# Kernel optimization log

Measured on AMD Instinct MI355X. Metric: run time of the kernel, lower is better.

## Reference

```python
import jax, jax.numpy as jnp
import numpy as np

N_RAYS = 32768
N_SAMPLES = 1048576
HID = 64
STEP = 0.0005


def _mlp(x, W1, b1, W2, b2, W3, b3):
    h = jax.nn.relu(x @ W1 + b1)
    h = jax.nn.relu(h @ W2 + b2)
    return h @ W3 + b3


def setup_inputs() -> dict:
    key = jax.random.key(0)
    ks = jax.random.split(key, 12)
    rays_o = jax.random.normal(ks[0], (N_RAYS, 3), jnp.float32)
    rays_d = jax.random.normal(ks[1], (N_RAYS, 3), jnp.float32)
    rays_d = rays_d / jnp.linalg.norm(rays_d, axis=-1, keepdims=True)
    t_starts = jax.random.uniform(ks[2], (N_SAMPLES,), jnp.float32, 0.0, 1.5)
    t_ends = t_starts + STEP
    ray_indices = jnp.sort(jax.random.randint(ks[3], (N_SAMPLES,), 0, N_RAYS, jnp.int32))
    def lin(k, fin, fout):
        return jax.random.normal(k, (fin, fout), jnp.float32) / np.sqrt(fin)
    return {
        'rays_o': rays_o, 'rays_d': rays_d,
        't_starts': t_starts, 't_ends': t_ends,
        'ray_indices': ray_indices,
        'W_d1': lin(ks[4], 3, HID), 'b_d1': jnp.zeros((HID,), jnp.float32),
        'W_d2': lin(ks[5], HID, HID), 'b_d2': jnp.zeros((HID,), jnp.float32),
        'W_d3': lin(ks[6], HID, 1), 'b_d3': jnp.zeros((1,), jnp.float32),
        'W_r1': lin(ks[7], 3, HID), 'b_r1': jnp.zeros((HID,), jnp.float32),
        'W_r2': lin(ks[8], HID, HID), 'b_r2': jnp.zeros((HID,), jnp.float32),
        'W_r3': lin(ks[9], HID, 3), 'b_r3': jnp.zeros((3,), jnp.float32),
    }


def reference(rays_o, rays_d, t_starts, t_ends, ray_indices,
              W_d1, b_d1, W_d2, b_d2, W_d3, b_d3,
              W_r1, b_r1, W_r2, b_r2, W_r3, b_r3):
    n_rays = rays_o.shape[0]
    mid = (t_starts + t_ends) * 0.5                      # [S]
    # gather ray origins/dirs per sample, compute positions
    positions = rays_o[ray_indices] + rays_d[ray_indices] * mid[:, None]  # [S,3]
    # density query (NGP decoder stand-in), softplus activation like trunc_exp family
    sigmas = jax.nn.softplus(_mlp(positions, W_d1, b_d1, W_d2, b_d2, W_d3, b_d3))[:, 0]  # [S]
    # render_weight_from_density: segment-wise exclusive cumsum of sigma*dt
    sigma_dt = sigmas * (t_ends - t_starts)              # [S]
    excl_global = jnp.cumsum(sigma_dt) - sigma_dt        # global exclusive cumsum
    per_ray = jax.ops.segment_sum(sigma_dt, ray_indices, num_segments=n_rays)  # [R]
    ray_excl = jnp.cumsum(per_ray) - per_ray             # exclusive cumsum over rays
    within_excl = excl_global - ray_excl[ray_indices]    # exclusive within each ray
    trans = jnp.exp(-within_excl)                        # transmittance
    alphas = 1.0 - jnp.exp(-sigma_dt)
    weights = trans * alphas
    # accumulate_along_rays (scatter-sum over ray_indices)
    opacities = jax.ops.segment_sum(weights, ray_indices, num_segments=n_rays)[:, None]  # [R,1]
    distances = jax.ops.segment_sum(weights * mid, ray_indices, num_segments=n_rays)[:, None]
    # rgb query
    rgbs = jax.nn.sigmoid(_mlp(positions, W_r1, b_r1, W_r2, b_r2, W_r3, b_r3))  # [S,3]
    w_sg = jax.lax.stop_gradient(weights)
    colors = jax.ops.segment_sum(w_sg[:, None] * rgbs, ray_indices, num_segments=n_rays)  # [R,3]
    # eval-mode background composition (nerf.training == False branch)
    rest = jax.lax.stop_gradient(1.0 - opacities)
    distances = distances + 5.0 * rest
    colors = colors + 0.5 * rest
    return colors, distances, opacities
```

## Files before the change

### kernel.cpp

```cpp
#include <hip/hip_runtime.h>
#include <hip/hip_bf16.h>
#include <math.h>

#define N_RAYS   32768
#define N_SAMP   1048576
#define HID      64
#define ITERS    4
#define BLK_HALF 1024
#define BLK_A    (2*BLK_HALF)

typedef short bf8 __attribute__((ext_vector_type(8)));
typedef float f4  __attribute__((ext_vector_type(4)));

union BF8U { bf8 v; unsigned u[4]; };

static __device__ __forceinline__ unsigned bfbits(float x) {
    union { __bf16 h; unsigned short s; } c; c.h = (__bf16)x; return (unsigned)c.s;
}
static __device__ __forceinline__ unsigned pk2(float a, float b) {
#if __has_builtin(__builtin_amdgcn_cvt_pk_bf16_f32)
    return __builtin_bit_cast(unsigned, __builtin_amdgcn_cvt_pk_bf16_f32(a, b));
#else
    return bfbits(a) | (bfbits(b) << 16);
#endif
}
static __device__ __forceinline__ unsigned pk2r(float a, float b) {
    return pk2(fmaxf(a, 0.f), fmaxf(b, 0.f));
}
static __device__ __forceinline__ f4 mfma16(bf8 a, bf8 b, f4 c) {
    return __builtin_amdgcn_mfma_f32_16x16x32_bf16(a, b, c, 0, 0, 0);
}

#define FRAG_SLOTS 14
#define BIAS_SLOTS 5

__global__ __launch_bounds__(128) void prep_frags(
    const float* __restrict__ Wd1, const float* __restrict__ bd1,
    const float* __restrict__ Wd2, const float* __restrict__ bd2,
    const float* __restrict__ Wd3, const float* __restrict__ bd3,
    const float* __restrict__ Wr1, const float* __restrict__ br1,
    const float* __restrict__ Wr2, const float* __restrict__ br2,
    const float* __restrict__ Wr3, const float* __restrict__ br3,
    uint4* __restrict__ fragbuf, float4* __restrict__ biasbuf)
{
    const int tid  = threadIdx.x;
    if (tid >= 128) return;
    const int net  = tid >> 6;
    const int lane = tid & 63;
    const int q    = lane >> 4;
    const int n    = lane & 15;
    const int qn   = n >> 2, rn = n & 3;
    const int rt   = n & 3;

    const float* W1 = net ? Wr1 : Wd1;  const float* b1 = net ? br1 : bd1;
    const float* W2 = net ? Wr2 : Wd2;  const float* b2 = net ? br2 : bd2;
    const float* W3 = net ? Wr3 : Wd3;  const float* b3 = net ? br3 : bd3;
    const int    nc = net ? 3 : 1;
    const int    ch = net ? (rt < 3 ? rt : 2) : 0;

    uint4*  fb = fragbuf + net * (FRAG_SLOTS * 64);
    float4* bb = biasbuf + net * (BIAS_SLOTS * 64);

    for (int t = 0; t < 4; ++t) {
        const int row = 8*qn + 4*(t&1) + rn + 32*(t>>1);
        uint4 f;
        f.x = pk2(W1[row],       W1[HID+row]);
        f.y = pk2(W1[2*HID+row], b1[row]);
        f.z = 0u; f.w = 0u;
        fb[t*64 + lane] = f;
    }
    for (int t = 0; t < 4; ++t) {
        const int row = 8*qn + 4*(t&1) + rn + 32*(t>>1);
        for (int s = 0; s < 2; ++s) {
            unsigned u[4];
            for (int dw = 0; dw < 4; ++dw) {
                const int k = 8*q + 2*dw + 32*s;
                u[dw] = pk2(W2[k*HID+row], W2[(k+1)*HID+row]);
            }
            fb[(4 + 2*t + s)*64 + lane] = make_uint4(u[0], u[1], u[2], u[3]);
        }
    }
    for (int s = 0; s < 2; ++s) {
        unsigned u[4];
        for (int dw = 0; dw < 4; ++dw) {
            const int kg = 32*s + 8*q + 2*dw;
            u[dw] = pk2(W3[kg*nc + ch], W3[(kg+1)*nc + ch]);
        }
        fb[(12 + s)*64 + lane] = make_uint4(u[0], u[1], u[2], u[3]);
    }
    for (int t = 0; t < 4; ++t) {
        float4 f;
        f.x = b2[8*q + 4*(t&1) + 0 + 32*(t>>1)];
        f.y = b2[8*q + 4*(t&1) + 1 + 32*(t>>1)];
        f.z = b2[8*q + 4*(t&1) + 2 + 32*(t>>1)];
        f.w = b2[8*q + 4*(t&1) + 3 + 32*(t>>1)];
        bb[t*64 + lane] = f;
    }
    {
        float4 f;
        f.x = net ? b3[0] : b3[0];
        f.y = net ? b3[1] : b3[0];
        f.z = net ? b3[2] : b3[0];
        f.w = net ? b3[2] : b3[0];
        bb[4*64 + lane] = f;
    }
}

__global__ __launch_bounds__(256) void seg_starts(
    const int* __restrict__ ray_idx, int* __restrict__ start)
{
    int s = blockIdx.x * blockDim.x + threadIdx.x;
    if (s >= N_SAMP) return;
    int b = ray_idx[s];
    int a = (s == 0) ? -1 : ray_idx[s-1];
    for (int r = a + 1; r <= b; ++r) start[r] = s;
    if (s == N_SAMP - 1)
        for (int r = b + 1; r <= N_RAYS; ++r) start[r] = N_SAMP;
}

__global__ __launch_bounds__(256) void pass_a(
    const float* __restrict__ rays_o, const float* __restrict__ rays_d,
    const float* __restrict__ t_starts, const float* __restrict__ t_ends,
    const int*   __restrict__ ray_idx,
    const uint4* __restrict__ fragbuf, const float4* __restrict__ biasbuf,
    float* __restrict__ ws_sd, float* __restrict__ ws_r,
    float* __restrict__ ws_g,  float* __restrict__ ws_b)
{
    const bool is_rgb = blockIdx.x >= BLK_HALF;
    const int  blk    = is_rgb ? (blockIdx.x - BLK_HALF) : blockIdx.x;
    const int  lane   = threadIdx.x & 63;
    const int  wv     = ((blk << 8) + threadIdx.x) >> 6;
    const int  q      = lane >> 4;

    const uint4*  fb = fragbuf + (is_rgb ? FRAG_SLOTS*64 : 0);
    const float4* bb = biasbuf + (is_rgb ? BIAS_SLOTS*64 : 0);

    bf8 a1[4];
    #pragma unroll
    for (int t = 0; t < 4; ++t)
        a1[t] = __builtin_bit_cast(bf8, fb[t*64 + lane]);
    bf8 a2[4][2];
    #pragma unroll
    for (int t = 0; t < 4; ++t)
        #pragma unroll
        for (int s = 0; s < 2; ++s)
            a2[t][s] = __builtin_bit_cast(bf8, fb[(4 + 2*t + s)*64 + lane]);
    bf8 a3[2];
    #pragma unroll
    for (int s = 0; s < 2; ++s)
        a3[s] = __builtin_bit_cast(bf8, fb[(12 + s)*64 + lane]);
    f4 bias2[4];
    #pragma unroll
    for (int t = 0; t < 4; ++t)
        bias2[t] = __builtin_bit_cast(f4, bb[t*64 + lane]);
    f4 bias3 = __builtin_bit_cast(f4, bb[4*64 + lane]);

    const int base0 = wv * (ITERS * 64);

    unsigned p01_[ITERS], p23_[ITERS];
    float    dt_[ITERS];
    #pragma unroll
    for (int it = 0; it < ITERS; ++it) {
        const int smp = base0 + it * 64 + lane;
        const float ts = t_starts[smp], te = t_ends[smp];
        const int   ri = ray_idx[smp];
        const float mid = 0.5f*(ts+te);
        dt_[it] = te - ts;
        const float px = rays_o[3*ri+0] + rays_d[3*ri+0]*mid;
        const float py = rays_o[3*ri+1] + rays_d[3*ri+1]*mid;
        const float pz = rays_o[3*ri+2] + rays_d[3*ri+2]*mid;
        p01_[it] = pk2(px, py);
        p23_[it] = pk2(pz, 1.0f);
    }

    #pragma unroll
    for (int it = 0; it < ITERS; ++it) {
        const int smp = base0 + it * 64 + lane;

        f4 mine = {0.f, 0.f, 0.f, 0.f};

        #pragma unroll
        for (int u = 0; u < 4; ++u) {
            BF8U xb;
            xb.u[0] = (q == u) ? p01_[it] : 0u;
            xb.u[1] = (q == u) ? p23_[it] : 0u;
            xb.u[2] = 0u; xb.u[3] = 0u;

            const f4 zero = {0.f, 0.f, 0.f, 0.f};
            f4 d1[4];
            #pragma unroll
            for (int t = 0; t < 4; ++t) d1[t] = mfma16(a1[t], xb.v, zero);

            bf8 bf2[2];
            #pragma unroll
            for (int s = 0; s < 2; ++s) {
                BF8U p;
                p.u[0] = pk2r(d1[2*s][0],   d1[2*s][1]);
                p.u[1] = pk2r(d1[2*s][2],   d1[2*s][3]);
                p.u[2] = pk2r(d1[2*s+1][0], d1[2*s+1][1]);
                p.u[3] = pk2r(d1[2*s+1][2], d1[2*s+1][3]);
                bf2[s] = p.v;
            }

            f4 d2[4];
            #pragma unroll
            for (int t = 0; t < 4; ++t) {
                f4 a = bias2[t];
                a = mfma16(a2[t][0], bf2[0], a);
                a = mfma16(a2[t][1], bf2[1], a);
                d2[t] = a;
            }

            bf8 bf3[2];
            #pragma unroll
            for (int s = 0; s < 2; ++s) {
                BF8U p;
                p.u[0] = pk2r(d2[2*s][0],   d2[2*s][1]);
                p.u[1] = pk2r(d2[2*s][2],   d2[2*s][3]);
                p.u[2] = pk2r(d2[2*s+1][0], d2[2*s+1][1]);
                p.u[3] = pk2r(d2[2*s+1][2], d2[2*s+1][3]);
                bf3[s] = p.v;
            }

            f4 c3 = bias3;
            c3 = mfma16(a3[0], bf3[0], c3);
            c3 = mfma16(a3[1], bf3[1], c3);

            if (q == u) mine = c3;
        }

        if (!is_rgb) {
            const float sg = mine[0];
            const float sp = fmaxf(sg, 0.f) + __logf(1.f + __expf(-fabsf(sg)));
            ws_sd[smp] = sp * dt_[it];
        } else {
            ws_r[smp] = __builtin_amdgcn_rcpf(1.f + __expf(-mine[0]));
            ws_g[smp] = __builtin_amdgcn_rcpf(1.f + __expf(-mine[1]));
            ws_b[smp] = __builtin_amdgcn_rcpf(1.f + __expf(-mine[2]));
        }
    }
}

__global__ __launch_bounds__(256) void pass_b(
    const float* __restrict__ t_starts, const float* __restrict__ t_ends,
    const float* __restrict__ ws_sd, const float* __restrict__ ws_r,
    const float* __restrict__ ws_g,  const float* __restrict__ ws_b,
    const int* __restrict__ start, float* __restrict__ out)
{
    const int lane = threadIdx.x & 63;
    const int wv   = (blockIdx.x * blockDim.x + threadIdx.x) >> 6;
    const int half = lane >> 5;
    const int l32  = lane & 31;
    const int r    = 2*wv + half;
    if (r >= N_RAYS) return;

    int s0 = start[r], s1 = start[r+1];
    s0 = min(max(s0, 0), N_SAMP);
    s1 = min(max(s1, s0), N_SAMP);

    float cum = 0.f, opac = 0.f, dist = 0.f, c0 = 0.f, c1 = 0.f, c2 = 0.f;

    for (int base = s0; base < s1; base += 32) {
        int s = base + l32;
        bool ok = s < s1;
        float sd  = ok ? ws_sd[s] : 0.f;
        float vr  = ok ? ws_r[s]  : 0.f;
        float vg  = ok ? ws_g[s]  : 0.f;
        float vb  = ok ? ws_b[s]  : 0.f;
        float mid = ok ? 0.5f*(t_starts[s] + t_ends[s]) : 0.f;

        float x = sd;
        #pragma unroll
        for (int off = 1; off < 32; off <<= 1) {
            float y = __shfl_up(x, off, 32);
            if (l32 >= off) x += y;
        }
        float incl = cum + x;
        float excl = incl - sd;
        float w = __expf(-excl) - __expf(-incl);
        dist += w*mid; c0 += w*vr; c1 += w*vg; c2 += w*vb;

        float tot = __shfl(x, 31, 32);
        opac += __expf(-cum) - __expf(-(cum + tot));
        cum  += tot;
    }

    #pragma unroll
    for (int off = 16; off > 0; off >>= 1) {
        dist += __shfl_xor(dist, off, 32);
        c0   += __shfl_xor(c0,   off, 32);
        c1   += __shfl_xor(c1,   off, 32);
        c2   += __shfl_xor(c2,   off, 32);
    }

    if (l32 == 0) {
        float rest = 1.f - opac;
        out[r*3 + 0] = c0 + 0.5f * rest;
        out[r*3 + 1] = c1 + 0.5f * rest;
        out[r*3 + 2] = c2 + 0.5f * rest;
        out[3*N_RAYS + r] = dist + 5.f * rest;
        out[4*N_RAYS + r] = opac;
    }
}

extern "C" void kernel_launch(void* const* d_in, const int* in_sizes, int n_in,
                              void* d_out, int out_size, void* d_ws, size_t ws_size,
                              hipStream_t stream) {
    const float* rays_o   = (const float*)d_in[0];
    const float* rays_d   = (const float*)d_in[1];
    const float* t_starts = (const float*)d_in[2];
    const float* t_ends   = (const float*)d_in[3];
    const int*   ray_idx  = (const int*)  d_in[4];
    const float* Wd1 = (const float*)d_in[5];  const float* bd1 = (const float*)d_in[6];
    const float* Wd2 = (const float*)d_in[7];  const float* bd2 = (const float*)d_in[8];
    const float* Wd3 = (const float*)d_in[9];  const float* bd3 = (const float*)d_in[10];
    const float* Wr1 = (const float*)d_in[11]; const float* br1 = (const float*)d_in[12];
    const float* Wr2 = (const float*)d_in[13]; const float* br2 = (const float*)d_in[14];
    const float* Wr3 = (const float*)d_in[15]; const float* br3 = (const float*)d_in[16];

    float* ws_sd = (float*)d_ws;
    float* ws_r  = ws_sd + N_SAMP;
    float* ws_g  = ws_r  + N_SAMP;
    float* ws_b  = ws_g  + N_SAMP;
    char*  p     = (char*)(ws_b + N_SAMP);
    int*    start   = (int*)p;
    uint4*  fragbuf = (uint4*)(p + ((N_RAYS+1)*4 + 255 & ~255));
    float4* biasbuf = (float4*)(fragbuf + 2*FRAG_SLOTS*64);
    float*  out     = (float*)d_out;

    hipLaunchKernelGGL(prep_frags, dim3(1), dim3(128), 0, stream,
                       Wd1, bd1, Wd2, bd2, Wd3, bd3,
                       Wr1, br1, Wr2, br2, Wr3, br3, fragbuf, biasbuf);

    hipLaunchKernelGGL(seg_starts, dim3((N_SAMP + 255)/256), dim3(256), 0, stream,
                       ray_idx, start);

    hipLaunchKernelGGL(pass_a, dim3(BLK_A), dim3(256), 0, stream,
                       rays_o, rays_d, t_starts, t_ends, ray_idx,
                       fragbuf, biasbuf, ws_sd, ws_r, ws_g, ws_b);

    hipLaunchKernelGGL(pass_b, dim3((N_RAYS/2 * 64) / 256), dim3(256), 0, stream,
                       t_starts, t_ends, ws_sd, ws_r, ws_g, ws_b, start, out);
}
```

Baseline: 155.1 us.

## Fuse segment-start computation into MLP pass and drop separate kernel

Removes the seg_starts kernel and computes the per-ray start offsets inside the density half of pass_a, using a wave shuffle to get the previous ray index. This saves a kernel launch and a separate pass over ray_idx. The sample loop is also no longer split into a prefetch phase plus a compute phase: each iteration loads and computes in place with unroll 1, and launch bounds now ask for 3 blocks per CU. The aim is lower register pressure and higher occupancy, at the cost of less load prefetching ahead of the MFMA work.

```diff
diff --git a/kernel.cpp b/kernel.cpp
--- a/kernel.cpp
+++ b/kernel.cpp
@@ -98,7 +98,7 @@
     }
     {
         float4 f;
-        f.x = net ? b3[0] : b3[0];
+        f.x = b3[0];
         f.y = net ? b3[1] : b3[0];
         f.z = net ? b3[2] : b3[0];
         f.w = net ? b3[2] : b3[0];
@@ -106,25 +106,14 @@
     }
 }
 
-__global__ __launch_bounds__(256) void seg_starts(
-    const int* __restrict__ ray_idx, int* __restrict__ start)
-{
-    int s = blockIdx.x * blockDim.x + threadIdx.x;
-    if (s >= N_SAMP) return;
-    int b = ray_idx[s];
-    int a = (s == 0) ? -1 : ray_idx[s-1];
-    for (int r = a + 1; r <= b; ++r) start[r] = s;
-    if (s == N_SAMP - 1)
-        for (int r = b + 1; r <= N_RAYS; ++r) start[r] = N_SAMP;
-}
-
-__global__ __launch_bounds__(256) void pass_a(
+__global__ __launch_bounds__(256, 3) void pass_a(
     const float* __restrict__ rays_o, const float* __restrict__ rays_d,
     const float* __restrict__ t_starts, const float* __restrict__ t_ends,
     const int*   __restrict__ ray_idx,
     const uint4* __restrict__ fragbuf, const float4* __restrict__ biasbuf,
     float* __restrict__ ws_sd, float* __restrict__ ws_r,
-    float* __restrict__ ws_g,  float* __restrict__ ws_b)
+    float* __restrict__ ws_g,  float* __restrict__ ws_b,
+    int* __restrict__ start)
 {
     const bool is_rgb = blockIdx.x >= BLK_HALF;
     const int  blk    = is_rgb ? (blockIdx.x - BLK_HALF) : blockIdx.x;
@@ -157,33 +146,34 @@
 
     const int base0 = wv * (ITERS * 64);
 
-    unsigned p01_[ITERS], p23_[ITERS];
-    float    dt_[ITERS];
-    #pragma unroll
+    #pragma unroll 1
     for (int it = 0; it < ITERS; ++it) {
         const int smp = base0 + it * 64 + lane;
+
         const float ts = t_starts[smp], te = t_ends[smp];
         const int   ri = ray_idx[smp];
-        const float mid = 0.5f*(ts+te);
-        dt_[it] = te - ts;
+        const float mid = 0.5f*(ts+te), dt = te - ts;
         const float px = rays_o[3*ri+0] + rays_d[3*ri+0]*mid;
         const float py = rays_o[3*ri+1] + rays_d[3*ri+1]*mid;
         const float pz = rays_o[3*ri+2] + rays_d[3*ri+2]*mid;
-        p01_[it] = pk2(px, py);
-        p23_[it] = pk2(pz, 1.0f);
-    }
-
-    #pragma unroll
-    for (int it = 0; it < ITERS; ++it) {
-        const int smp = base0 + it * 64 + lane;
+        const unsigned p01 = pk2(px, py);
+        const unsigned p23 = pk2(pz, 1.0f);
+
+        if (!is_rgb) {
+            int rp = __shfl_up(ri, 1, 64);
+            if (lane == 0) rp = (smp == 0) ? -1 : ray_idx[smp-1];
+            for (int rr = rp + 1; rr <= ri; ++rr) start[rr] = smp;
+            if (smp == N_SAMP - 1)
+                for (int rr = ri + 1; rr <= N_RAYS; ++rr) start[rr] = N_SAMP;
+        }
 
         f4 mine = {0.f, 0.f, 0.f, 0.f};
 
         #pragma unroll
         for (int u = 0; u < 4; ++u) {
             BF8U xb;
-            xb.u[0] = (q == u) ? p01_[it] : 0u;
-            xb.u[1] = (q == u) ? p23_[it] : 0u;
+            xb.u[0] = (q == u) ? p01 : 0u;
+            xb.u[1] = (q == u) ? p23 : 0u;
             xb.u[2] = 0u; xb.u[3] = 0u;
 
             const f4 zero = {0.f, 0.f, 0.f, 0.f};
@@ -232,7 +222,7 @@
         if (!is_rgb) {
             const float sg = mine[0];
             const float sp = fmaxf(sg, 0.f) + __logf(1.f + __expf(-fabsf(sg)));
-            ws_sd[smp] = sp * dt_[it];
+            ws_sd[smp] = sp * dt;
         } else {
             ws_r[smp] = __builtin_amdgcn_rcpf(1.f + __expf(-mine[0]));
             ws_g[smp] = __builtin_amdgcn_rcpf(1.f + __expf(-mine[1]));
@@ -324,7 +314,7 @@
     float* ws_b  = ws_g  + N_SAMP;
     char*  p     = (char*)(ws_b + N_SAMP);
     int*    start   = (int*)p;
-    uint4*  fragbuf = (uint4*)(p + ((N_RAYS+1)*4 + 255 & ~255));
+    uint4*  fragbuf = (uint4*)(p + (((N_RAYS+1)*4 + 255) & ~255));
     float4* biasbuf = (float4*)(fragbuf + 2*FRAG_SLOTS*64);
     float*  out     = (float*)d_out;
 
@@ -332,12 +322,9 @@
                        Wd1, bd1, Wd2, bd2, Wd3, bd3,
                        Wr1, br1, Wr2, br2, Wr3, br3, fragbuf, biasbuf);
 
-    hipLaunchKernelGGL(seg_starts, dim3((N_SAMP + 255)/256), dim3(256), 0, stream,
-                       ray_idx, start);
-
     hipLaunchKernelGGL(pass_a, dim3(BLK_A), dim3(256), 0, stream,
                        rays_o, rays_d, t_starts, t_ends, ray_idx,
-                       fragbuf, biasbuf, ws_sd, ws_r, ws_g, ws_b);
+                       fragbuf, biasbuf, ws_sd, ws_r, ws_g, ws_b, start);
 
     hipLaunchKernelGGL(pass_b, dim3((N_RAYS/2 * 64) / 256), dim3(256), 0, stream,
                        t_starts, t_ends, ws_sd, ws_r, ws_g, ws_b, start, out);
```

Measured after the change: 147.4 us. 1.05x faster.
